# Kernel optimization log

Hardware: AMD Instinct MI355X
Metric: run time of the kernel (lower is better)

Reference implementation:

```python
import jax, jax.numpy as jnp
import numpy as np

DIM, HEADS, HDIM, B, L = 2048, 16, 128, 2, 2048

def setup_inputs() -> dict:
    key = jax.random.key(0)
    ks = jax.random.split(key, 7)
    s = 1.0 / np.sqrt(DIM)
    return {
        "x": jax.random.normal(ks[0], (B, L, DIM), jnp.float32),
        "rope_emb": jax.random.uniform(ks[1], (L, HDIM), jnp.float32),
        "wq": jax.random.normal(ks[2], (DIM, DIM), jnp.float32) * s,
        "wk": jax.random.normal(ks[3], (DIM, DIM), jnp.float32) * s,
        "wv": jax.random.normal(ks[4], (DIM, DIM), jnp.float32) * s,
        "wo": jax.random.normal(ks[5], (DIM, DIM), jnp.float32) * s,
        "bo": jnp.zeros((DIM,), jnp.float32),
    }

def _rotate_half(x):
    x1, x2 = jnp.split(x, 2, axis=-1)
    return jnp.concatenate((-x2, x1), axis=-1)

def reference(x, rope_emb, wq, wk, wv, wo, bo):
    Bq, Lq, D = x.shape
    # projections; torch Linear: y = x @ W.T, weights here stored as [out,in]
    q = jnp.einsum("bld,ed->ble", x, wq).reshape(Bq, Lq, HEADS, HDIM).transpose(0, 2, 1, 3)
    k = jnp.einsum("bld,ed->ble", x, wk).reshape(Bq, Lq, HEADS, HDIM).transpose(0, 2, 1, 3)
    v = jnp.einsum("bld,ed->ble", x, wv).reshape(Bq, Lq, HEADS, HDIM).transpose(0, 2, 1, 3)
    cos = jnp.cos(rope_emb)[None, None]  # [1,1,L,hd]
    sin = jnp.sin(rope_emb)[None, None]
    q = q * cos + _rotate_half(q) * sin
    k = k * cos + _rotate_half(k) * sin
    scale = HDIM ** -0.5
    attn = jnp.einsum("bhqd,bhkd->bhqk", q, k) * scale
    attn = jax.nn.softmax(attn, axis=-1)
    out = jnp.einsum("bhqk,bhkd->bhqd", attn, v)
    out = out.transpose(0, 2, 1, 3).reshape(Bq, Lq, D)
    return jnp.einsum("bld,ed->ble", out, wo) + bo
```

## Files before the change

### kernel.cpp

```cpp
#include <hip/hip_runtime.h>
#include <hip/hip_bf16.h>
#include <stdint.h>

#define DIMS  2048
#define HEADS 16
#define HD    128
#define BATCH 2
#define SEQ   2048
#define MROWS (BATCH*SEQ)
#define QKVN  (3*DIMS)

using bf16x8 = __attribute__((ext_vector_type(8))) short;
using f32x4  = __attribute__((ext_vector_type(4))) float;
using f32x16 = __attribute__((ext_vector_type(16))) float;
using u16x4  = __attribute__((ext_vector_type(4))) unsigned short;

__device__ __forceinline__ unsigned short f2b(float f){
    __hip_bfloat16 h = __float2bfloat16(f);
    return *reinterpret_cast<unsigned short*>(&h);
}
__device__ __forceinline__ float b2f(unsigned short u){
    __hip_bfloat16 h;
    *reinterpret_cast<unsigned short*>(&h) = u;
    return __bfloat162float(h);
}
__device__ __forceinline__ unsigned int pkbf(float lo, float hi){
    return (unsigned int)f2b(lo) | ((unsigned int)f2b(hi) << 16);
}

__device__ __forceinline__ void glds16(const void* g, void* l){
    __builtin_amdgcn_global_load_lds(
        (const __attribute__((address_space(1))) unsigned int*)g,
        (__attribute__((address_space(3))) unsigned int*)l, 16, 0, 0);
}


__global__ void k_f32bf16(const float* __restrict__ src, unsigned short* __restrict__ dst, int n4){
    int i = blockIdx.x*blockDim.x + threadIdx.x;
    if (i >= n4) return;
    const float4 v = reinterpret_cast<const float4*>(src)[i];
    u16x4 o = { f2b(v.x), f2b(v.y), f2b(v.z), f2b(v.w) };
    *reinterpret_cast<u16x4*>(dst + 4*(size_t)i) = o;
}

__global__ void k_cossin(const float* __restrict__ r, float* __restrict__ c, float* __restrict__ s, int n){
    int i = blockIdx.x*blockDim.x + threadIdx.x;
    if (i >= n) return;
    float v = r[i];
    c[i] = cosf(v);
    s[i] = sinf(v);
}

__global__ void k_rope(unsigned short* __restrict__ qkv,
                       const float* __restrict__ ct, const float* __restrict__ st){
    const int idx = blockIdx.x*blockDim.x + threadIdx.x;
    const int d = idx & 63;
    const int h = (idx >> 6) & (HEADS-1);
    const int l = (idx >> 10) & (SEQ-1);
    const int b = idx >> 21;
    const float c0 = ct[l*HD + d],      s0 = st[l*HD + d];
    const float c1 = ct[l*HD + d + 64], s1 = st[l*HD + d + 64];
    unsigned short* row = qkv + (size_t)(b*SEQ + l)*QKVN + h*HD;
    {
        float x1 = b2f(row[d]), x2 = b2f(row[d+64]);
        row[d]    = f2b(x1*c0 - x2*s0);
        row[d+64] = f2b(x2*c1 + x1*s1);
    }
    {
        unsigned short* kr = row + DIMS;
        float x1 = b2f(kr[d]), x2 = b2f(kr[d+64]);
        kr[d]    = f2b(x1*c0 - x2*s0);
        kr[d+64] = f2b(x2*c1 + x1*s1);
    }
}

__global__ void k_vtrans(const unsigned short* __restrict__ qkv, unsigned short* __restrict__ vt){
    __shared__ unsigned short t[64*68];
    const int lt = blockIdx.x;
    const int dt = blockIdx.y;
    const int bh = blockIdx.z;
    const int b = bh >> 4, h = bh & 15;
    const int tid = threadIdx.x;
    const int l0 = lt << 6;
    #pragma unroll
    for (int it = 0; it < 4; ++it){
        const int c = tid + (it<<8);
        const int l = c >> 4;
        const int d4 = (c & 15) << 2;
        const u16x4 v = *reinterpret_cast<const u16x4*>(
            qkv + (size_t)(b*SEQ + l0 + l)*QKVN + 2*DIMS + h*HD + (dt<<6) + d4);
        *reinterpret_cast<u16x4*>(&t[l*68 + d4]) = v;
    }
    __syncthreads();
    #pragma unroll
    for (int it = 0; it < 4; ++it){
        const int c = tid + (it<<8);
        const int d = c >> 4;
        const int l4 = (c & 15) << 2;
        u16x4 o = { t[(l4+0)*68 + d], t[(l4+1)*68 + d], t[(l4+2)*68 + d], t[(l4+3)*68 + d] };
        *reinterpret_cast<u16x4*>(&vt[((size_t)bh*HD + (dt<<6) + d)*SEQ + l0 + l4]) = o;
    }
}


template<int FINAL>
__global__ __launch_bounds__(256) void k_gemm_bt(
    const unsigned short* __restrict__ A, const unsigned short* __restrict__ B,
    void* __restrict__ C, const float* __restrict__ bias, int M, int N, int K)
{
    __shared__ unsigned short lA[128*64];
    __shared__ unsigned short lB[128*64];
    const int tid  = threadIdx.x;
    const int lane = tid & 63;
    const int wave = tid >> 6;

    const int nbx = N >> 7;
    const int nwg = gridDim.x;
    const int cpx = nwg >> 3;
    const int bid = blockIdx.x;
    const int wg  = (bid & 7)*cpx + (bid >> 3);
    const int m0 = (wg / nbx) << 7;
    const int n0 = (wg % nbx) << 7;

    const int wr = (wave >> 1) << 6;
    const int wc = (wave & 1) << 6;

    f32x4 acc[4][4] = {};

    const int srow_base = (wave<<3) + (lane>>3);
    const int schunk = lane & 7;

    for (int k0 = 0; k0 < K; k0 += 64){
        #pragma unroll
        for (int i = 0; i < 4; ++i){
            const int row  = (i<<5) + srow_base;
            const int scol = k0 + ((schunk ^ (row & 7)) << 3);
            glds16(A + (size_t)(m0 + row)*K + scol, &lA[((i<<5) + (wave<<3)) << 6]);
            glds16(B + (size_t)(n0 + row)*K + scol, &lB[((i<<5) + (wave<<3)) << 6]);
        }
        __syncthreads();
        #pragma unroll
        for (int ks = 0; ks < 2; ++ks){
            bf16x8 af[4], bfr[4];
            const int colbase = (ks<<5) + ((lane>>4)<<3);
            #pragma unroll
            for (int mi = 0; mi < 4; ++mi){
                const int row = wr + (mi<<4) + (lane & 15);
                af[mi] = *reinterpret_cast<const bf16x8*>(&lA[(row<<6) + (colbase ^ ((row&7)<<3))]);
            }
            #pragma unroll
            for (int ni = 0; ni < 4; ++ni){
                const int row = wc + (ni<<4) + (lane & 15);
                bfr[ni] = *reinterpret_cast<const bf16x8*>(&lB[(row<<6) + (colbase ^ ((row&7)<<3))]);
            }
            #pragma unroll
            for (int mi = 0; mi < 4; ++mi)
                #pragma unroll
                for (int ni = 0; ni < 4; ++ni)
                    acc[mi][ni] = __builtin_amdgcn_mfma_f32_16x16x32_bf16(af[mi], bfr[ni], acc[mi][ni], 0, 0, 0);
        }
        __syncthreads();
    }

    const int r0 = (lane >> 4) << 2;
    const int cn = lane & 15;
    #pragma unroll
    for (int mi = 0; mi < 4; ++mi)
        #pragma unroll
        for (int r = 0; r < 4; ++r){
            const int gm = m0 + wr + (mi<<4) + r0 + r;
            #pragma unroll
            for (int ni = 0; ni < 4; ++ni){
                const int gn = n0 + wc + (ni<<4) + cn;
                const float v = acc[mi][ni][r];
                if (FINAL)
                    reinterpret_cast<float*>(C)[(size_t)gm*N + gn] = v + bias[gn];
                else
                    reinterpret_cast<unsigned short*>(C)[(size_t)gm*N + gn] = f2b(v);
            }
        }
}


union U8 { unsigned int w[4]; bf16x8 v; };

__global__ __launch_bounds__(512, 2) void k_attn(
    const unsigned short* __restrict__ qkv, const unsigned short* __restrict__ vt,
    unsigned short* __restrict__ aout)
{
    __shared__ unsigned short lK[2][64*128];
    __shared__ unsigned short lV[2][128*64];
    __shared__ unsigned short lO[8*32*132];

    const int tid  = threadIdx.x;
    const int lane = tid & 63;
    const int wave = tid >> 6;
    const int lq   = lane & 31;
    const int hi   = lane >> 5;
    const int bh = blockIdx.y;
    const int b = bh >> 4, h = bh & 15;
    const int q0w = (blockIdx.x << 8) + (wave << 5);

    const unsigned short* Kb = qkv + (size_t)b*SEQ*QKVN + DIMS + h*HD;
    const unsigned short* Vb = vt + (size_t)bh*HD*SEQ;

    bf16x8 qf[8];
    {
        const float qscale = 0.08838834764831845f * 1.4426950408889634f;
        const unsigned short* qp = qkv + (size_t)(b*SEQ + q0w + lq)*QKVN + h*HD + (hi<<3);
        #pragma unroll
        for (int ks = 0; ks < 8; ++ks){
            bf16x8 tv = *reinterpret_cast<const bf16x8*>(qp + (ks<<4));
            #pragma unroll
            for (int j = 0; j < 8; ++j)
                tv[j] = (short)f2b(b2f((unsigned short)tv[j]) * qscale);
            qf[ks] = tv;
        }
    }

    float m_run = -3e38f, l_run = 0.f;
    f32x16 oacc[4] = {};

    #define STAGE(pb, kv0) do { \
        _Pragma("unroll") \
        for (int i = 0; i < 2; ++i){ \
            const int kr = (wave<<3) + (i<<2) + (lane>>4); \
            glds16(Kb + (size_t)((kv0) + kr)*QKVN + (((lane&15) ^ (kr&7))<<3), \
                   &lK[pb][((wave<<3) + (i<<2))<<7]); \
            const int dr = (wave<<4) + (i<<3) + (lane>>3); \
            glds16(Vb + (size_t)dr*SEQ + (kv0) + (((lane&7) ^ (dr&7))<<3), \
                   &lV[pb][((wave<<4) + (i<<3))<<6]); \
        } \
    } while(0)

    int buf = 0;
    STAGE(0, 0);
    __syncthreads();

    for (int t = 0; t < SEQ/64; ++t){
        if (t < SEQ/64 - 1) STAGE(buf^1, (t+1)*64);

        const unsigned short* Kbuf = &lK[buf][0];
        const unsigned short* Vbuf = &lV[buf][0];

        f32x16 st0 = {}, st1 = {};
        #pragma unroll
        for (int ks = 0; ks < 8; ++ks){
            const int col = (((ks<<1) + hi) ^ (lq & 7)) << 3;
            bf16x8 k0 = *reinterpret_cast<const bf16x8*>(&Kbuf[(lq<<7) + col]);
            bf16x8 k1 = *reinterpret_cast<const bf16x8*>(&Kbuf[((32+lq)<<7) + col]);
            st0 = __builtin_amdgcn_mfma_f32_32x32x16_bf16(k0, qf[ks], st0, 0, 0, 0);
            st1 = __builtin_amdgcn_mfma_f32_32x32x16_bf16(k1, qf[ks], st1, 0, 0, 0);
        }

        float tmax = st0[0];
        #pragma unroll
        for (int r = 1; r < 16; ++r) tmax = fmaxf(tmax, st0[r]);
        #pragma unroll
        for (int r = 0; r < 16; ++r) tmax = fmaxf(tmax, st1[r]);
        tmax = fmaxf(tmax, __shfl_xor(tmax, 32));
        const float mnew = fmaxf(m_run, tmax);
        const float al = __builtin_amdgcn_exp2f(m_run - mnew);
        m_run = mnew;
        float tsum = 0.f;
        #pragma unroll
        for (int r = 0; r < 16; ++r){ float p = __builtin_amdgcn_exp2f(st0[r] - mnew); st0[r] = p; tsum += p; }
        #pragma unroll
        for (int r = 0; r < 16; ++r){ float p = __builtin_amdgcn_exp2f(st1[r] - mnew); st1[r] = p; tsum += p; }
        tsum += __shfl_xor(tsum, 32);
        l_run = l_run*al + tsum;
        #pragma unroll
        for (int dt = 0; dt < 4; ++dt) oacc[dt] *= al;

        bf16x8 pf[4];
        #define MAKEPF(dA, dB, SV) do { \
            unsigned int a0 = pkbf(SV[0],SV[1]),  b0 = pkbf(SV[2],SV[3]); \
            unsigned int c0 = pkbf(SV[4],SV[5]),  d0 = pkbf(SV[6],SV[7]); \
            unsigned int a1 = pkbf(SV[8],SV[9]),  b1 = pkbf(SV[10],SV[11]); \
            unsigned int c1 = pkbf(SV[12],SV[13]),d1 = pkbf(SV[14],SV[15]); \
            unsigned int ax0 = __shfl_xor(a0,32), bx0 = __shfl_xor(b0,32); \
            unsigned int cx0 = __shfl_xor(c0,32), dx0 = __shfl_xor(d0,32); \
            unsigned int ax1 = __shfl_xor(a1,32), bx1 = __shfl_xor(b1,32); \
            unsigned int cx1 = __shfl_xor(c1,32), dx1 = __shfl_xor(d1,32); \
            U8 u; \
            u.w[0] = hi ? cx0 : a0;  u.w[1] = hi ? dx0 : b0; \
            u.w[2] = hi ? c0 : ax0;  u.w[3] = hi ? d0 : bx0; \
            dA = u.v; \
            u.w[0] = hi ? cx1 : a1;  u.w[1] = hi ? dx1 : b1; \
            u.w[2] = hi ? c1 : ax1;  u.w[3] = hi ? d1 : bx1; \
            dB = u.v; \
        } while(0)
        MAKEPF(pf[0], pf[1], st0);
        MAKEPF(pf[2], pf[3], st1);
        #undef MAKEPF

        #pragma unroll
        for (int dt = 0; dt < 4; ++dt){
            const int rowv = (dt<<5) + lq;
            #pragma unroll
            for (int f = 0; f < 4; ++f){
                const int col = (((f<<1) + hi) ^ (lq & 7)) << 3;
                bf16x8 vf = *reinterpret_cast<const bf16x8*>(&Vbuf[(rowv<<6) + col]);
                oacc[dt] = __builtin_amdgcn_mfma_f32_32x32x16_bf16(vf, pf[f], oacc[dt], 0, 0, 0);
            }
        }

        __syncthreads();
        buf ^= 1;
    }
    #undef STAGE

    const float rl = 1.0f / l_run;
    unsigned short* oL = lO + wave*(32*132);
    #pragma unroll
    for (int dt = 0; dt < 4; ++dt)
        #pragma unroll
        for (int g = 0; g < 4; ++g){
            u16x4 w = { f2b(oacc[dt][g*4+0]*rl), f2b(oacc[dt][g*4+1]*rl),
                        f2b(oacc[dt][g*4+2]*rl), f2b(oacc[dt][g*4+3]*rl) };
            *reinterpret_cast<u16x4*>(&oL[lq*132 + (dt<<5) + (hi<<2) + (g<<3)]) = w;
        }
    #pragma unroll
    for (int i = 0; i < 16; ++i){
        const int q = (i<<1) + hi;
        u16x4 w = *reinterpret_cast<const u16x4*>(&oL[q*132 + (lq<<2)]);
        *reinterpret_cast<u16x4*>(&aout[(size_t)(b*SEQ + q0w + q)*DIMS + h*HD + (lq<<2)]) = w;
    }
}


extern "C" void kernel_launch(void* const* d_in, const int* in_sizes, int n_in,
                              void* d_out, int out_size, void* d_ws, size_t ws_size,
                              hipStream_t stream)
{
    const float* x    = (const float*)d_in[0];
    const float* rope = (const float*)d_in[1];
    const float* wq   = (const float*)d_in[2];
    const float* wk   = (const float*)d_in[3];
    const float* wv   = (const float*)d_in[4];
    const float* wo   = (const float*)d_in[5];
    const float* bo   = (const float*)d_in[6];
    float* out = (float*)d_out;

    char* ws = (char*)d_ws;
    unsigned short* x_bf   = (unsigned short*)(ws + 0);
    unsigned short* wqkv   = (unsigned short*)(ws + 16777216);
    unsigned short* wo_bf  = (unsigned short*)(ws + 41943040);
    float*          cos_t  = (float*)(ws + 50331648);
    float*          sin_t  = (float*)(ws + 51380224);
    unsigned short* qkv    = (unsigned short*)(ws + 52428800);
    unsigned short* vt     = (unsigned short*)(ws + 16777216);
    unsigned short* a_out  = (unsigned short*)(ws + 0);

    k_f32bf16<<<8192, 256, 0, stream>>>(x,  x_bf,              2097152);
    k_f32bf16<<<4096, 256, 0, stream>>>(wq, wqkv,              1048576);
    k_f32bf16<<<4096, 256, 0, stream>>>(wk, wqkv + 4194304,    1048576);
    k_f32bf16<<<4096, 256, 0, stream>>>(wv, wqkv + 8388608,    1048576);
    k_f32bf16<<<4096, 256, 0, stream>>>(wo, wo_bf,             1048576);
    k_cossin <<<1024, 256, 0, stream>>>(rope, cos_t, sin_t, SEQ*HD);

    k_gemm_bt<0><<<(MROWS/128)*(QKVN/128), 256, 0, stream>>>(x_bf, wqkv, qkv, nullptr, MROWS, QKVN, DIMS);

    k_rope<<<16384, 256, 0, stream>>>(qkv, cos_t, sin_t);

    k_vtrans<<<dim3(SEQ/64, HD/64, BATCH*HEADS), 256, 0, stream>>>(qkv, vt);

    k_attn<<<dim3(SEQ/256, BATCH*HEADS), 512, 0, stream>>>(qkv, vt, a_out);

    k_gemm_bt<1><<<(MROWS/128)*(DIMS/128), 256, 0, stream>>>(a_out, wo_bf, out, bo, MROWS, DIMS, DIMS);
}
```

Before: 309.8 us.

## Add 256x256-tile 8-wave pipelined GEMM for the QKV projection

Replaces the 128x128 QKV projection GEMM with a new 256x256-tile kernel that uses 512 threads, swizzled LDS staging via direct global-to-LDS loads, and a four-quadrant schedule. Loads for later k-tiles are interleaved with the MFMA quadrants under explicit barriers and waitcnts, and the kernel also remaps workgroup IDs and raises MFMA priority. The larger tiles are meant to raise arithmetic intensity and hide memory latency behind compute. In exchange it uses a lot of LDS and registers, which risks low occupancy and makes the hand-written scheduling fragile.

```diff
diff --git a/kernel.cpp b/kernel.cpp
--- a/kernel.cpp
+++ b/kernel.cpp
@@ -179,6 +179,139 @@
                     reinterpret_cast<unsigned short*>(C)[(size_t)gm*N + gn] = f2b(v);
             }
         }
+}
+
+
+__device__ __forceinline__ void stg256(const unsigned short* __restrict__ src, int row0, int k0,
+                                       unsigned short* dstregion, int wave, int lane, int Kld){
+    #pragma unroll
+    for (int i = 0; i < 2; ++i){
+        const int r  = (i<<6) + (wave<<3) + (lane>>3);
+        const int cc = (lane&7) ^ (r&7);
+        glds16(src + (size_t)(row0 + r)*Kld + k0 + (cc<<3), dstregion + (((i<<6)+(wave<<3))<<6));
+    }
+}
+
+__global__ __launch_bounds__(512, 2) void k_gemm256(
+    const unsigned short* __restrict__ A, const unsigned short* __restrict__ B,
+    unsigned short* __restrict__ C, int M, int N, int K)
+{
+    __shared__ unsigned short lA[2*2*128*64];
+    __shared__ unsigned short lB[2*2*128*64];
+
+    const int tid  = threadIdx.x;
+    const int lane = tid & 63;
+    const int wave = tid >> 6;
+    const int wm   = wave >> 2;
+    const int wn   = wave & 3;
+    const int nkt  = K >> 6;
+
+    const int nbx = N >> 8;
+    const int nwg = gridDim.x;
+    const int cpx = nwg >> 3;
+    const int wg  = (blockIdx.x & 7)*cpx + (blockIdx.x >> 3);
+    const int m0 = (wg / nbx) << 8;
+    const int n0 = (wg % nbx) << 8;
+
+    f32x4 acc[2][2][4][2] = {};
+
+#define REGION(LX, T, H) (&LX[(((((T)&1)<<1)+(H))<<13)])
+#define ST_A(T, H) do{ if ((T) < nkt) stg256(A, m0 + ((H)<<7), (T)<<6, REGION(lA,T,H), wave, lane, K); }while(0)
+#define ST_B(T, H) do{ if ((T) < nkt) stg256(B, n0 + ((H)<<7), (T)<<6, REGION(lB,T,H), wave, lane, K); }while(0)
+
+#define RD_A(DST, REG) do{ \
+    _Pragma("unroll") for (int mi=0;mi<4;++mi) _Pragma("unroll") for (int ks=0;ks<2;++ks){ \
+        const int rowh = (wm<<6) + (mi<<4) + (lane&15); \
+        const int c8 = (ks<<2) + (lane>>4); \
+        DST[mi][ks] = *reinterpret_cast<const bf16x8*>(&(REG)[(rowh<<6) + ((c8 ^ (rowh&7))<<3)]); \
+    } }while(0)
+#define RD_B(DST, REG) do{ \
+    _Pragma("unroll") for (int ni=0;ni<2;++ni) _Pragma("unroll") for (int ks=0;ks<2;++ks){ \
+        const int rowh = (wn<<5) + (ni<<4) + (lane&15); \
+        const int c8 = (ks<<2) + (lane>>4); \
+        DST[ni][ks] = *reinterpret_cast<const bf16x8*>(&(REG)[(rowh<<6) + ((c8 ^ (rowh&7))<<3)]); \
+    } }while(0)
+
+#define BARRIER() do{ __builtin_amdgcn_sched_barrier(0); __builtin_amdgcn_s_barrier(); \
+                      __builtin_amdgcn_sched_barrier(0); }while(0)
+
+#define MM16(QM, QN, AF, BF) do{ \
+    __builtin_amdgcn_s_setprio(1); \
+    _Pragma("unroll") for (int ks=0;ks<2;++ks) \
+    _Pragma("unroll") for (int mi=0;mi<4;++mi) \
+    _Pragma("unroll") for (int ni=0;ni<2;++ni) \
+        acc[QM][QN][mi][ni] = __builtin_amdgcn_mfma_f32_16x16x32_bf16(AF[mi][ks], BF[ni][ks], acc[QM][QN][mi][ni], 0,0,0); \
+    __builtin_amdgcn_s_setprio(0); \
+    }while(0)
+
+    ST_A(0,0); ST_B(0,1); ST_A(0,1); ST_B(0,0);
+    ST_A(1,0); ST_B(1,1); ST_A(1,1);
+    __builtin_amdgcn_sched_barrier(0);
+    asm volatile("s_waitcnt vmcnt(6)");
+    BARRIER();
+
+    for (int t = 0; t < nkt; ++t){
+        const unsigned short* rA0 = REGION(lA, t, 0);
+        const unsigned short* rA1 = REGION(lA, t, 1);
+        const unsigned short* rB0 = REGION(lB, t, 0);
+        const unsigned short* rB1 = REGION(lB, t, 1);
+
+        bf16x8 a0f[4][2], a1f[4][2], b0f[2][2], b1f[2][2];
+
+        RD_A(a0f, rA0);
+        RD_B(b0f, rB0);
+        ST_B(t+1, 0);
+        BARRIER();
+        MM16(0, 0, a0f, b0f);
+        BARRIER();
+
+        RD_B(b1f, rB1);
+        ST_A(t+2, 0);
+        BARRIER();
+        MM16(0, 1, a0f, b1f);
+        BARRIER();
+
+        RD_A(a1f, rA1);
+        ST_B(t+2, 1);
+        BARRIER();
+        MM16(1, 1, a1f, b1f);
+        BARRIER();
+
+        RD_B(b0f, rB0);
+        ST_A(t+2, 1);
+        BARRIER();
+        MM16(1, 0, a1f, b0f);
+        __builtin_amdgcn_sched_barrier(0);
+        if (t + 2 < nkt) { asm volatile("s_waitcnt vmcnt(6)"); }
+        else             { asm volatile("s_waitcnt vmcnt(0)"); }
+        BARRIER();
+    }
+
+#undef REGION
+#undef ST_A
+#undef ST_B
+#undef RD_A
+#undef RD_B
+#undef BARRIER
+#undef MM16
+
+    const int r0 = (lane >> 4) << 2;
+    const int cn = lane & 15;
+    #pragma unroll
+    for (int qm = 0; qm < 2; ++qm)
+      #pragma unroll
+      for (int qn = 0; qn < 2; ++qn)
+        #pragma unroll
+        for (int mi = 0; mi < 4; ++mi)
+          #pragma unroll
+          for (int rr = 0; rr < 4; ++rr){
+              const int gm = m0 + (qm<<7) + (wm<<6) + (mi<<4) + r0 + rr;
+              #pragma unroll
+              for (int ni = 0; ni < 2; ++ni){
+                  const int gn = n0 + (qn<<7) + (wn<<5) + (ni<<4) + cn;
+                  C[(size_t)gm*N + gn] = f2b(acc[qm][qn][mi][ni][rr]);
+              }
+          }
 }
 
 
@@ -359,7 +492,7 @@
     k_f32bf16<<<4096, 256, 0, stream>>>(wo, wo_bf,             1048576);
     k_cossin <<<1024, 256, 0, stream>>>(rope, cos_t, sin_t, SEQ*HD);
 
-    k_gemm_bt<0><<<(MROWS/128)*(QKVN/128), 256, 0, stream>>>(x_bf, wqkv, qkv, nullptr, MROWS, QKVN, DIMS);
+    k_gemm256<<<(MROWS/256)*(QKVN/256), 512, 0, stream>>>(x_bf, wqkv, qkv, MROWS, QKVN, DIMS);
 
     k_rope<<<16384, 256, 0, stream>>>(qkv, cos_t, sin_t);
 
```

Result: no change. 308.7 us (-0.3%).

## Replace GEMM with 256x128 tile, double-buffered LDS pipeline and 8 waves

Applied to the files above, without the earlier changes.

The projection GEMMs now use 512-thread blocks computing 256x128 output tiles. A and B are double-buffered in LDS, with staged global-to-LDS loads for future k-tiles overlapped with MFMA work. Fine-grained waitcnt, barriers and s_setprio interleave loads with compute. This targets the load-then-sync stall of the old single-buffered 128x128 kernel, at the cost of more LDS (96KB), fewer blocks, and a more fragile hand-scheduled pipeline.

```diff
diff --git a/kernel.cpp b/kernel.cpp
--- a/kernel.cpp
+++ b/kernel.cpp
@@ -103,76 +103,112 @@
 }
 
 
+__device__ __forceinline__ void stg128(const unsigned short* __restrict__ src, int row0, int k0,
+                                       unsigned short* dstregion, int wave, int lane, int Kld){
+    #pragma unroll
+    for (int i = 0; i < 2; ++i){
+        const int r  = (i<<6) + (wave<<3) + (lane>>3);
+        const int cc = (lane&7) ^ (r&7);
+        glds16(src + (size_t)(row0 + r)*Kld + k0 + (cc<<3), dstregion + (((i<<6)+(wave<<3))<<6));
+    }
+}
+
 template<int FINAL>
-__global__ __launch_bounds__(256) void k_gemm_bt(
+__global__ __launch_bounds__(512, 2) void k_gemm256b(
     const unsigned short* __restrict__ A, const unsigned short* __restrict__ B,
     void* __restrict__ C, const float* __restrict__ bias, int M, int N, int K)
 {
-    __shared__ unsigned short lA[128*64];
-    __shared__ unsigned short lB[128*64];
+    __shared__ unsigned short lA[2][2][128*64];
+    __shared__ unsigned short lB[2][128*64];
+
     const int tid  = threadIdx.x;
     const int lane = tid & 63;
     const int wave = tid >> 6;
+    const int wm   = wave >> 2;
+    const int wn   = wave & 3;
+    const int nkt  = K >> 6;
 
     const int nbx = N >> 7;
     const int nwg = gridDim.x;
     const int cpx = nwg >> 3;
-    const int bid = blockIdx.x;
-    const int wg  = (bid & 7)*cpx + (bid >> 3);
-    const int m0 = (wg / nbx) << 7;
+    const int wg  = (blockIdx.x & 7)*cpx + (blockIdx.x >> 3);
+    const int m0 = (wg / nbx) << 8;
     const int n0 = (wg % nbx) << 7;
 
-    const int wr = (wave >> 1) << 6;
-    const int wc = (wave & 1) << 6;
-
-    f32x4 acc[4][4] = {};
-
-    const int srow_base = (wave<<3) + (lane>>3);
-    const int schunk = lane & 7;
-
-    for (int k0 = 0; k0 < K; k0 += 64){
-        #pragma unroll
-        for (int i = 0; i < 4; ++i){
-            const int row  = (i<<5) + srow_base;
-            const int scol = k0 + ((schunk ^ (row & 7)) << 3);
-            glds16(A + (size_t)(m0 + row)*K + scol, &lA[((i<<5) + (wave<<3)) << 6]);
-            glds16(B + (size_t)(n0 + row)*K + scol, &lB[((i<<5) + (wave<<3)) << 6]);
-        }
-        __syncthreads();
-        #pragma unroll
-        for (int ks = 0; ks < 2; ++ks){
-            bf16x8 af[4], bfr[4];
-            const int colbase = (ks<<5) + ((lane>>4)<<3);
-            #pragma unroll
-            for (int mi = 0; mi < 4; ++mi){
-                const int row = wr + (mi<<4) + (lane & 15);
-                af[mi] = *reinterpret_cast<const bf16x8*>(&lA[(row<<6) + (colbase ^ ((row&7)<<3))]);
-            }
-            #pragma unroll
-            for (int ni = 0; ni < 4; ++ni){
-                const int row = wc + (ni<<4) + (lane & 15);
-                bfr[ni] = *reinterpret_cast<const bf16x8*>(&lB[(row<<6) + (colbase ^ ((row&7)<<3))]);
-            }
-            #pragma unroll
-            for (int mi = 0; mi < 4; ++mi)
-                #pragma unroll
-                for (int ni = 0; ni < 4; ++ni)
-                    acc[mi][ni] = __builtin_amdgcn_mfma_f32_16x16x32_bf16(af[mi], bfr[ni], acc[mi][ni], 0, 0, 0);
-        }
-        __syncthreads();
-    }
+    f32x4 acc[2][4][2] = {};
+
+#define ST_A(T, H) do{ if ((T) < nkt) stg128(A, m0 + ((H)<<7), (T)<<6, &lA[(T)&1][H][0], wave, lane, K); }while(0)
+#define ST_B(T)    do{ if ((T) < nkt) stg128(B, n0,            (T)<<6, &lB[(T)&1][0],    wave, lane, K); }while(0)
+
+#define RD_A(REG) do{ \
+    _Pragma("unroll") for (int mi=0;mi<4;++mi) _Pragma("unroll") for (int ks=0;ks<2;++ks){ \
+        const int rowh = (wm<<6) + (mi<<4) + (lane&15); \
+        const int c8 = (ks<<2) + (lane>>4); \
+        af[mi][ks] = *reinterpret_cast<const bf16x8*>(&(REG)[(rowh<<6) + ((c8 ^ (rowh&7))<<3)]); \
+    } }while(0)
+#define RD_B(REG) do{ \
+    _Pragma("unroll") for (int ni=0;ni<2;++ni) _Pragma("unroll") for (int ks=0;ks<2;++ks){ \
+        const int rowh = (wn<<5) + (ni<<4) + (lane&15); \
+        const int c8 = (ks<<2) + (lane>>4); \
+        bf[ni][ks] = *reinterpret_cast<const bf16x8*>(&(REG)[(rowh<<6) + ((c8 ^ (rowh&7))<<3)]); \
+    } }while(0)
+
+#define MM(H) do{ \
+    __builtin_amdgcn_s_setprio(1); \
+    _Pragma("unroll") for (int ks=0;ks<2;++ks) \
+    _Pragma("unroll") for (int mi=0;mi<4;++mi) \
+    _Pragma("unroll") for (int ni=0;ni<2;++ni) \
+        acc[H][mi][ni] = __builtin_amdgcn_mfma_f32_16x16x32_bf16(af[mi][ks], bf[ni][ks], acc[H][mi][ni], 0,0,0); \
+    __builtin_amdgcn_s_setprio(0); \
+    }while(0)
+
+    ST_A(0,0); ST_B(0); ST_A(0,1);
+    ST_A(1,0); ST_B(1);
+    asm volatile("s_waitcnt vmcnt(4)" ::: "memory");
+    __builtin_amdgcn_s_barrier();
+    __builtin_amdgcn_sched_barrier(0);
+
+    for (int t = 0; t < nkt; ++t){
+        const int p = t & 1;
+        bf16x8 af[4][2], bf[2][2];
+
+        RD_A(lA[p][0]);
+        RD_B(lB[p]);
+        ST_A(t+1, 1);
+        __builtin_amdgcn_s_barrier();
+        MM(0);
+        __builtin_amdgcn_s_barrier();
+
+        RD_A(lA[p][1]);
+        ST_A(t+2, 0);
+        ST_B(t+2);
+        __builtin_amdgcn_s_barrier();
+        MM(1);
+        if (t + 2 < nkt) { asm volatile("s_waitcnt vmcnt(4)" ::: "memory"); }
+        else             { asm volatile("s_waitcnt vmcnt(0)" ::: "memory"); }
+        __builtin_amdgcn_s_barrier();
+        __builtin_amdgcn_sched_barrier(0);
+    }
+
+#undef ST_A
+#undef ST_B
+#undef RD_A
+#undef RD_B
+#undef MM
 
     const int r0 = (lane >> 4) << 2;
     const int cn = lane & 15;
     #pragma unroll
-    for (int mi = 0; mi < 4; ++mi)
-        #pragma unroll
-        for (int r = 0; r < 4; ++r){
-            const int gm = m0 + wr + (mi<<4) + r0 + r;
+    for (int h = 0; h < 2; ++h)
+      #pragma unroll
+      for (int mi = 0; mi < 4; ++mi)
+        #pragma unroll
+        for (int rr = 0; rr < 4; ++rr){
+            const int gm = m0 + (h<<7) + (wm<<6) + (mi<<4) + r0 + rr;
             #pragma unroll
-            for (int ni = 0; ni < 4; ++ni){
-                const int gn = n0 + wc + (ni<<4) + cn;
-                const float v = acc[mi][ni][r];
+            for (int ni = 0; ni < 2; ++ni){
+                const int gn = n0 + (wn<<5) + (ni<<4) + cn;
+                const float v = acc[h][mi][ni][rr];
                 if (FINAL)
                     reinterpret_cast<float*>(C)[(size_t)gm*N + gn] = v + bias[gn];
                 else
@@ -359,7 +395,7 @@
     k_f32bf16<<<4096, 256, 0, stream>>>(wo, wo_bf,             1048576);
     k_cossin <<<1024, 256, 0, stream>>>(rope, cos_t, sin_t, SEQ*HD);
 
-    k_gemm_bt<0><<<(MROWS/128)*(QKVN/128), 256, 0, stream>>>(x_bf, wqkv, qkv, nullptr, MROWS, QKVN, DIMS);
+    k_gemm256b<0><<<(MROWS/256)*(QKVN/128), 512, 0, stream>>>(x_bf, wqkv, qkv, nullptr, MROWS, QKVN, DIMS);
 
     k_rope<<<16384, 256, 0, stream>>>(qkv, cos_t, sin_t);
 
@@ -367,5 +403,5 @@
 
     k_attn<<<dim3(SEQ/256, BATCH*HEADS), 512, 0, stream>>>(qkv, vt, a_out);
 
-    k_gemm_bt<1><<<(MROWS/128)*(DIMS/128), 256, 0, stream>>>(a_out, wo_bf, out, bo, MROWS, DIMS, DIMS);
-}
+    k_gemm256b<1><<<(MROWS/256)*(DIMS/128), 512, 0, stream>>>(a_out, wo_bf, out, bo, MROWS, DIMS, DIMS);
+}
```

Measured after the change: 313.6 us. About the same (+1.2%).
